# Performance work log

Measured on AMD Instinct MI355X. Metric: run time of the kernel, lower is better.

Reference implementation:

```python
import jax, jax.numpy as jnp
import numpy as np

EPS = 1e-5
TOP_K = 2


def _dwconv3x3(x, w):
    # depthwise 3x3, stride 1, padding 1 (SAME)
    return jax.lax.conv_general_dilated(
        x, w, window_strides=(1, 1), padding='SAME',
        feature_group_count=x.shape[1],
        dimension_numbers=('NCHW', 'OIHW', 'NCHW'))


def _bn(x, g, b, m, v):
    # inference-mode BatchNorm2d
    s = g / jnp.sqrt(v + EPS)
    return x * s[None, :, None, None] + (b - m * s)[None, :, None, None]


def setup_inputs() -> dict:
    key = jax.random.key(0)
    ks = jax.random.split(key, 26)
    Bsz, D, H = 16, 384, 32
    S, E, HID = 64, 8, 768
    n, u = jax.random.normal, jax.random.uniform
    inp = {}
    inp['x'] = n(ks[0], (Bsz, D, H, H), jnp.float32)
    inp['dw1_w'] = n(ks[1], (D, 1, 3, 3)) * 0.1
    inp['bn1_g'] = u(ks[2], (D,), minval=0.5, maxval=1.5)
    inp['bn1_b'] = n(ks[3], (D,)) * 0.1
    inp['bn1_m'] = n(ks[4], (D,)) * 0.1
    inp['bn1_v'] = u(ks[5], (D,), minval=0.5, maxval=1.5)
    inp['dw2_w'] = n(ks[6], (D, 1, 3, 3)) * 0.1
    inp['bn2_g'] = u(ks[7], (D,), minval=0.5, maxval=1.5)
    inp['bn2_b'] = n(ks[8], (D,)) * 0.1
    inp['bn2_m'] = n(ks[9], (D,)) * 0.1
    inp['bn2_v'] = u(ks[10], (D,), minval=0.5, maxval=1.5)
    inp['ln_w'] = u(ks[11], (D,), minval=0.5, maxval=1.5)
    inp['ln_b'] = n(ks[12], (D,)) * 0.1
    inp['bcdt_w'] = n(ks[13], (3 * S, D)) * 0.02
    inp['dws_w'] = n(ks[14], (3 * S, 1, 3, 3)) * 0.1
    inp['hproj_w'] = n(ks[15], (D, D)) * 0.02
    inp['A'] = u(ks[16], (S,), minval=1.0, maxval=16.0)
    inp['gate_w'] = n(ks[17], (E, D)) * 0.02
    inp['gate_b'] = n(ks[18], (E,)) * 0.02
    inp['w1'] = n(ks[19], (E, HID, D)) * 0.02
    inp['b1'] = n(ks[20], (E, HID)) * 0.02
    inp['w2'] = n(ks[21], (E, D, HID)) * 0.02
    inp['b2'] = n(ks[22], (E, D)) * 0.02
    inp['w3'] = n(ks[23], (E, HID, D)) * 0.02
    inp['b3'] = n(ks[24], (E, HID)) * 0.02
    return inp


def reference(x, dw1_w, bn1_g, bn1_b, bn1_m, bn1_v, dw2_w, bn2_g, bn2_b, bn2_m,
              bn2_v, ln_w, ln_b, bcdt_w, dws_w, hproj_w, A, gate_w, gate_b,
              w1, b1, w2, b2, w3, b3):
    Bsz, D, H, W = x.shape
    L = H * W
    S = A.shape[0]
    E = gate_w.shape[0]
    # x = x + dwconv1(x)
    x = x + _bn(_dwconv3x3(x, dw1_w), bn1_g, bn1_b, bn1_m, bn1_v)
    x_prev = x
    # LayerNorm1D over channel dim of (B, C, L)
    xf = x.reshape(Bsz, D, L)
    mu = xf.mean(axis=1, keepdims=True)
    var = xf.var(axis=1, keepdims=True)
    xn = (xf - mu) / jnp.sqrt(var + EPS) * ln_w[None, :, None] + ln_b[None, :, None]
    # Slim_SSD mixer
    bcdt = jnp.einsum('cd,bdl->bcl', bcdt_w, xn)            # 1x1 conv1d
    bcdt = _dwconv3x3(bcdt.reshape(Bsz, 3 * S, H, W), dws_w).reshape(Bsz, 3 * S, L)
    Bm, Cm, dt = jnp.split(bcdt, 3, axis=1)                  # each (B, S, L)
    Am = jax.nn.softmax(dt + A[None, :, None], axis=-1)      # softmax over L
    h = jnp.einsum('bdl,bsl->bds', xn, Am * Bm)              # (B, D, S)
    h = jax.nn.silu(jnp.einsum('ed,bds->bes', hproj_w, h))   # h_proj + SiLU
    y = jnp.einsum('bes,bsl->bel', h, Cm).reshape(Bsz, D, H, W)
    x = x_prev + y
    # x = x + dwconv2(x)
    x = x + _bn(_dwconv3x3(x, dw2_w), bn2_g, bn2_b, bn2_m, bn2_v)
    # SparseMoE (TopkRouter, eval mode, filter_radio=0 -> mask==1, bias buffer==0)
    t = x.transpose(0, 2, 3, 1).reshape(-1, D)               # (N, D) tokens
    N = t.shape[0]
    logits = t @ gate_w.T + gate_b                           # (N, E)
    vals, idx = jax.lax.top_k(logits, TOP_K)
    probs = jax.nn.softmax(vals, axis=1)                     # softmax over top-k logits
    wfull = jnp.zeros((N, E), t.dtype).at[jnp.arange(N)[:, None], idx].set(probs)
    ymoe = jnp.zeros_like(t)
    for e in range(E):
        he = jax.nn.silu(t @ w1[e].T + b1[e]) * (t @ w3[e].T + b3[e])
        ymoe = ymoe + (he @ w2[e].T + b2[e]) * wfull[:, e:e + 1]
    x = x + ymoe.reshape(Bsz, H, W, D).transpose(0, 3, 1, 2)
    # dropout is identity in eval mode
    return (x, h)
```

## Files before the change

kernel.cpp:

```cpp
#include <hip/hip_runtime.h>
#include <hip/hip_bf16.h>

#define BSZ 16
#define DCH 384
#define LSP 1024
#define SST 64
#define NEXP 8
#define HID 768
#define NTOK 16384
#define MOE_MAXT 520

#define OFF_X1    0ULL
#define OFF_XN    25165824ULL
#define OFF_BCDT  50331648ULL
#define OFF_BCDTC 62914560ULL
#define OFF_H     75497472ULL
#define OFF_X2    77070336ULL
#define OFF_META  102236160ULL
#define OFF_LOGITS (OFF_META)
#define OFF_PROBS  (OFF_META +  524288ULL)
#define OFF_IDX    (OFF_META +  655360ULL)
#define OFF_CNT    (OFF_META +  786432ULL)
#define OFF_FILL   (OFF_META +  786464ULL)
#define OFF_OFFS   (OFF_META +  786496ULL)
#define OFF_TOFF   (OFF_META +  786560ULL)
#define OFF_LTOK   (OFF_META +  786624ULL)
#define OFF_LP     (OFF_META +  917696ULL)
#define OFF_TPOS   (OFF_META + 1048768ULL)
#define OFF_HE    0ULL
#define OFF_T16   OFF_BCDT
#define OFF_W1B   OFF_BCDTC
#define OFF_W3B   (OFF_BCDTC + 4718592ULL)
#define OFF_W2B   (OFF_BCDTC + 9437184ULL)
#define OFF_YMOE  OFF_X2
#define OFF_HPRE  OFF_X2

typedef __attribute__((ext_vector_type(8))) short bf16x8;
typedef __attribute__((ext_vector_type(4))) float f32x4;
typedef __attribute__((ext_vector_type(4))) unsigned short u16x4;

__device__ __forceinline__ unsigned short f2bf(float f) {
  union { float f; unsigned int u; } x; x.f = f;
  unsigned int r = (x.u + 0x7fffu + ((x.u >> 16) & 1u)) >> 16;
  return (unsigned short)r;
}
__device__ __forceinline__ float bf2f(unsigned short s) {
  union { unsigned int u; float f; } x; x.u = ((unsigned int)s) << 16; return x.f;
}

__global__ void k_dwbnres(const float* __restrict__ x, const float* __restrict__ w,
                          const float* __restrict__ g, const float* __restrict__ bb,
                          const float* __restrict__ mm, const float* __restrict__ vv,
                          float* __restrict__ out, int C) {
  int bc = blockIdx.x;
  int c = bc % C;
  __shared__ float tile[34 * 34];
  const float* img = x + (size_t)bc * 1024;
  for (int i = threadIdx.x; i < 34 * 34; i += 256) tile[i] = 0.f;
  __syncthreads();
  for (int i = threadIdx.x; i < 1024; i += 256) {
    int r = i >> 5, cc = i & 31;
    tile[(r + 1) * 34 + (cc + 1)] = img[i];
  }
  __syncthreads();
  float w0 = w[c*9+0], w1 = w[c*9+1], w2 = w[c*9+2], w3 = w[c*9+3], w4 = w[c*9+4],
        w5 = w[c*9+5], w6 = w[c*9+6], w7 = w[c*9+7], w8 = w[c*9+8];
  bool res = (g != nullptr);
  float scale = 1.f, bias = 0.f;
  if (res) { float s = g[c] * rsqrtf(vv[c] + 1e-5f); scale = s; bias = bb[c] - mm[c] * s; }
  for (int i = threadIdx.x; i < 1024; i += 256) {
    int r = i >> 5, cc = i & 31;
    const float* t0 = &tile[r * 34 + cc];
    float acc = t0[0]*w0 + t0[1]*w1 + t0[2]*w2
              + t0[34]*w3 + t0[35]*w4 + t0[36]*w5
              + t0[68]*w6 + t0[69]*w7 + t0[70]*w8;
    float o = res ? (t0[35] + acc * scale + bias) : acc;
    out[(size_t)bc * 1024 + i] = o;
  }
}

__global__ void k_layernorm(const float* __restrict__ x, const float* __restrict__ lw,
                            const float* __restrict__ lb, float* __restrict__ xn) {
  int lane = threadIdx.x & 63;
  int slice = threadIdx.x >> 6;
  int pos0 = blockIdx.x * 64;
  int b = pos0 >> 10;
  int l = (pos0 & 1023) + lane;
  const float* xb = x + (size_t)b * DCH * LSP + l;
  float s = 0.f, s2 = 0.f;
  for (int d = slice * 96; d < slice * 96 + 96; d++) {
    float v = xb[(size_t)d * LSP];
    s += v; s2 += v * v;
  }
  __shared__ float red[2][4][64];
  red[0][slice][lane] = s; red[1][slice][lane] = s2;
  __syncthreads();
  if (slice == 0) {
    s  = red[0][0][lane] + red[0][1][lane] + red[0][2][lane] + red[0][3][lane];
    s2 = red[1][0][lane] + red[1][1][lane] + red[1][2][lane] + red[1][3][lane];
    float mu = s * (1.f / 384.f);
    float var = s2 * (1.f / 384.f) - mu * mu;
    red[0][0][lane] = mu;
    red[1][0][lane] = rsqrtf(var + 1e-5f);
  }
  __syncthreads();
  float mu = red[0][0][lane], rs = red[1][0][lane];
  float* xnb = xn + (size_t)b * DCH * LSP + l;
  for (int d = slice * 96; d < slice * 96 + 96; d++) {
    float v = xb[(size_t)d * LSP];
    xnb[(size_t)d * LSP] = (v - mu) * rs * lw[d] + lb[d];
  }
}

__global__ void k_bcdt(const float* __restrict__ xn, const float* __restrict__ wt,
                       float* __restrict__ out) {
  int lt = blockIdx.x, ct = blockIdx.y, b = blockIdx.z;
  __shared__ float wsm[64][33];
  __shared__ float xs[32][129];
  int lg = threadIdx.x & 31, cg = threadIdx.x >> 5;
  float acc[8][4];
  for (int i = 0; i < 8; i++) for (int j = 0; j < 4; j++) acc[i][j] = 0.f;
  const float* xb = xn + (size_t)b * DCH * LSP + lt * 128;
  for (int d0 = 0; d0 < 384; d0 += 32) {
    for (int i = threadIdx.x; i < 2048; i += 256) {
      int c = i >> 5, dd = i & 31;
      wsm[c][dd] = wt[(size_t)(ct * 64 + c) * 384 + d0 + dd];
    }
    for (int i = threadIdx.x; i < 4096; i += 256) {
      int dd = i >> 7, ll = i & 127;
      xs[dd][ll] = xb[(size_t)(d0 + dd) * LSP + ll];
    }
    __syncthreads();
    for (int dd = 0; dd < 32; dd++) {
      float xv[4];
      #pragma unroll
      for (int il = 0; il < 4; il++) xv[il] = xs[dd][lg + 32 * il];
      #pragma unroll
      for (int ic = 0; ic < 8; ic++) {
        float wv = wsm[cg + 8 * ic][dd];
        #pragma unroll
        for (int il = 0; il < 4; il++) acc[ic][il] += wv * xv[il];
      }
    }
    __syncthreads();
  }
  for (int ic = 0; ic < 8; ic++)
    for (int il = 0; il < 4; il++)
      out[(size_t)b * 196608 + (size_t)(ct * 64 + cg + 8 * ic) * 1024 + lt * 128 + lg + 32 * il] = acc[ic][il];
}

__global__ void k_softmax(float* __restrict__ bc, const float* __restrict__ Av) {
  int b = blockIdx.x >> 6, s = blockIdx.x & 63;
  float* row = bc + (size_t)b * 196608 + (size_t)(128 + s) * 1024;
  float a = Av[s];
  int t = threadIdx.x;
  float v[4]; float mx = -3.0e38f;
  #pragma unroll
  for (int i = 0; i < 4; i++) { v[i] = row[t + 256 * i] + a; mx = fmaxf(mx, v[i]); }
  #pragma unroll
  for (int off = 32; off >= 1; off >>= 1) mx = fmaxf(mx, __shfl_xor(mx, off));
  __shared__ float redm[4], reds[4];
  if ((t & 63) == 0) redm[t >> 6] = mx;
  __syncthreads();
  mx = fmaxf(fmaxf(redm[0], redm[1]), fmaxf(redm[2], redm[3]));
  float sm = 0.f;
  #pragma unroll
  for (int i = 0; i < 4; i++) { v[i] = __expf(v[i] - mx); sm += v[i]; }
  #pragma unroll
  for (int off = 32; off >= 1; off >>= 1) sm += __shfl_xor(sm, off);
  if ((t & 63) == 0) reds[t >> 6] = sm;
  __syncthreads();
  sm = reds[0] + reds[1] + reds[2] + reds[3];
  float inv = 1.f / sm;
  #pragma unroll
  for (int i = 0; i < 4; i++) row[t + 256 * i] = v[i] * inv;
}

__global__ void k_h(const float* __restrict__ xn, const float* __restrict__ bc,
                    float* __restrict__ h) {
  int dt_ = blockIdx.x, ls = blockIdx.y, b = blockIdx.z;
  __shared__ float xs[64][65];
  __shared__ float ab[64][65];
  int tid = threadIdx.x;
  int sg4 = tid & 15, dg4 = tid >> 4;
  float acc[4][4];
  #pragma unroll
  for (int i = 0; i < 4; i++)
    #pragma unroll
    for (int j = 0; j < 4; j++) acc[i][j] = 0.f;
  const float* Bm = bc + (size_t)b * 196608;
  const float* Am = Bm + 131072;
  const float* xb = xn + (size_t)b * DCH * LSP + (size_t)(dt_ * 64) * LSP;
  for (int l0 = ls * 128; l0 < ls * 128 + 128; l0 += 64) {
    for (int i = tid; i < 4096; i += 256) {
      int r = i >> 6, ll = i & 63;
      xs[r][ll] = xb[(size_t)r * LSP + l0 + ll];
      ab[r][ll] = Am[(size_t)r * 1024 + l0 + ll] * Bm[(size_t)r * 1024 + l0 + ll];
    }
    __syncthreads();
    for (int ll = 0; ll < 64; ll++) {
      float xv[4], av[4];
      #pragma unroll
      for (int i = 0; i < 4; i++) xv[i] = xs[dg4 * 4 + i][ll];
      #pragma unroll
      for (int j = 0; j < 4; j++) av[j] = ab[sg4 * 4 + j][ll];
      #pragma unroll
      for (int i = 0; i < 4; i++)
        #pragma unroll
        for (int j = 0; j < 4; j++) acc[i][j] += xv[i] * av[j];
    }
    __syncthreads();
  }
  float* hb = h + (size_t)b * DCH * SST + (size_t)(dt_ * 64) * 64;
  #pragma unroll
  for (int i = 0; i < 4; i++)
    #pragma unroll
    for (int j = 0; j < 4; j++)
      atomicAdd(&hb[(size_t)(dg4 * 4 + i) * 64 + sg4 * 4 + j], acc[i][j]);
}

__global__ void k_hproj(const float* __restrict__ h, const float* __restrict__ pw,
                        float* __restrict__ hpre) {
  int et = blockIdx.x, ks = blockIdx.y, b = blockIdx.z;
  __shared__ float hs[64][65];
  __shared__ float ps[64][65];
  int tid = threadIdx.x;
  int sg4 = tid & 15, eg4 = tid >> 4;
  float acc[4][4];
  #pragma unroll
  for (int i = 0; i < 4; i++)
    #pragma unroll
    for (int j = 0; j < 4; j++) acc[i][j] = 0.f;
  for (int d0 = ks * 128; d0 < ks * 128 + 128; d0 += 64) {
    for (int i = tid; i < 4096; i += 256) {
      int r = i >> 6, cc = i & 63;
      hs[r][cc] = h[(size_t)b * DCH * SST + (size_t)(d0 + r) * 64 + cc];
      ps[r][cc] = pw[(size_t)(et * 64 + r) * 384 + d0 + cc];
    }
    __syncthreads();
    for (int dd = 0; dd < 64; dd++) {
      float pv[4], hv[4];
      #pragma unroll
      for (int i = 0; i < 4; i++) pv[i] = ps[eg4 * 4 + i][dd];
      #pragma unroll
      for (int j = 0; j < 4; j++) hv[j] = hs[dd][sg4 * 4 + j];
      #pragma unroll
      for (int i = 0; i < 4; i++)
        #pragma unroll
        for (int j = 0; j < 4; j++) acc[i][j] += pv[i] * hv[j];
    }
    __syncthreads();
  }
  float* hb = hpre + (size_t)b * DCH * SST + (size_t)(et * 64) * 64;
  #pragma unroll
  for (int i = 0; i < 4; i++)
    #pragma unroll
    for (int j = 0; j < 4; j++)
      atomicAdd(&hb[(size_t)(eg4 * 4 + i) * 64 + sg4 * 4 + j], acc[i][j]);
}

__global__ void k_silu(const float* __restrict__ hpre, float* __restrict__ h2) {
  int i = blockIdx.x * 256 + threadIdx.x;
  float4 v = ((const float4*)hpre)[i];
  v.x = v.x / (1.f + __expf(-v.x));
  v.y = v.y / (1.f + __expf(-v.y));
  v.z = v.z / (1.f + __expf(-v.z));
  v.w = v.w / (1.f + __expf(-v.w));
  ((float4*)h2)[i] = v;
}

__global__ void k_y(const float* __restrict__ h2, const float* __restrict__ bc,
                    const float* __restrict__ x1, float* __restrict__ x2) {
  int lt = blockIdx.x, dt_ = blockIdx.y, b = blockIdx.z;
  __shared__ float hss[32][65];
  __shared__ float cs[64][129];
  int lg = threadIdx.x & 31, dg = threadIdx.x >> 5;
  float acc[4][4];
  for (int i = 0; i < 4; i++) for (int j = 0; j < 4; j++) acc[i][j] = 0.f;
  for (int i = threadIdx.x; i < 2048; i += 256) {
    int r = i >> 6, cc = i & 63;
    hss[r][cc] = h2[(size_t)b * DCH * SST + (size_t)(dt_ * 32 + r) * 64 + cc];
  }
  const float* Cm = bc + (size_t)b * 196608 + 65536;
  for (int i = threadIdx.x; i < 8192; i += 256) {
    int ss = i >> 7, ll = i & 127;
    cs[ss][ll] = Cm[(size_t)ss * 1024 + lt * 128 + ll];
  }
  __syncthreads();
  for (int ss = 0; ss < 64; ss++) {
    float cv[4];
    #pragma unroll
    for (int il = 0; il < 4; il++) cv[il] = cs[ss][lg + 32 * il];
    #pragma unroll
    for (int id = 0; id < 4; id++) {
      float hv = hss[dg * 4 + id][ss];
      #pragma unroll
      for (int il = 0; il < 4; il++) acc[id][il] += hv * cv[il];
    }
  }
  size_t base = (size_t)b * DCH * LSP + (size_t)(dt_ * 32) * LSP + lt * 128;
  for (int id = 0; id < 4; id++)
    for (int il = 0; il < 4; il++) {
      size_t o = base + (size_t)(dg * 4 + id) * LSP + lg + 32 * il;
      x2[o] = x1[o] + acc[id][il];
    }
}

__global__ void k_router(const float* __restrict__ x3, const float* __restrict__ gw,
                         const float* __restrict__ gb, float* __restrict__ logits) {
  __shared__ float xs[64][65];
  __shared__ float gs[8][64];
  int blk = blockIdx.x;
  int b = blk >> 4; int l0 = (blk & 15) * 64;
  int lg = threadIdx.x & 63, eg = threadIdx.x >> 6;
  float acc0 = 0.f, acc1 = 0.f;
  const float* xb = x3 + (size_t)b * DCH * LSP + l0;
  for (int d0 = 0; d0 < 384; d0 += 64) {
    for (int i = threadIdx.x; i < 4096; i += 256) {
      int dd = i >> 6, ll = i & 63;
      xs[dd][ll] = xb[(size_t)(d0 + dd) * LSP + ll];
    }
    for (int i = threadIdx.x; i < 512; i += 256) {
      int e = i >> 6, dd = i & 63;
      gs[e][dd] = gw[(size_t)e * 384 + d0 + dd];
    }
    __syncthreads();
    for (int dd = 0; dd < 64; dd++) {
      float xv = xs[dd][lg];
      acc0 += gs[eg][dd] * xv;
      acc1 += gs[eg + 4][dd] * xv;
    }
    __syncthreads();
  }
  int n = b * 1024 + l0 + lg;
  logits[(size_t)n * 8 + eg]     = acc0 + gb[eg];
  logits[(size_t)n * 8 + eg + 4] = acc1 + gb[eg + 4];
}

__global__ void k_topk(const float* __restrict__ logits, float* __restrict__ probs,
                       int* __restrict__ idx, int* __restrict__ cnt) {
  __shared__ int lcnt[8];
  if (threadIdx.x < 8) lcnt[threadIdx.x] = 0;
  __syncthreads();
  int n = blockIdx.x * 256 + threadIdx.x;
  float lv[8];
  for (int e = 0; e < 8; e++) lv[e] = logits[(size_t)n * 8 + e];
  int i1 = 0; float v1 = lv[0];
  for (int e = 1; e < 8; e++) if (lv[e] > v1) { v1 = lv[e]; i1 = e; }
  int i2 = -1; float v2 = -3.0e38f;
  for (int e = 0; e < 8; e++) { if (e == i1) continue; if (lv[e] > v2) { v2 = lv[e]; i2 = e; } }
  float p1 = 1.f / (1.f + __expf(v2 - v1));
  probs[n * 2] = p1; probs[n * 2 + 1] = 1.f - p1;
  idx[n * 2] = i1; idx[n * 2 + 1] = i2;
  atomicAdd(&lcnt[i1], 1); atomicAdd(&lcnt[i2], 1);
  __syncthreads();
  if (threadIdx.x < 8) atomicAdd(&cnt[threadIdx.x], lcnt[threadIdx.x]);
}

__global__ void k_offsets(const int* __restrict__ cnt, int* __restrict__ offs,
                          int* __restrict__ toff) {
  if (threadIdx.x == 0) {
    int a = 0, t = 0;
    for (int e = 0; e < 8; e++) {
      offs[e] = a; toff[e] = t;
      a += cnt[e]; t += (cnt[e] + 63) >> 6;
    }
    toff[8] = t;
  }
}

__global__ void k_build(const int* __restrict__ idx, const float* __restrict__ probs,
                        const int* __restrict__ offs, int* __restrict__ fill,
                        int* __restrict__ ltok, float* __restrict__ lp,
                        int* __restrict__ tpos) {
  __shared__ int lcnt[8], lbase[8];
  if (threadIdx.x < 8) lcnt[threadIdx.x] = 0;
  __syncthreads();
  int n = blockIdx.x * 256 + threadIdx.x;
  int e0 = idx[n * 2], e1 = idx[n * 2 + 1];
  int o0 = atomicAdd(&lcnt[e0], 1);
  int o1 = atomicAdd(&lcnt[e1], 1);
  __syncthreads();
  if (threadIdx.x < 8) lbase[threadIdx.x] = atomicAdd(&fill[threadIdx.x], lcnt[threadIdx.x]);
  __syncthreads();
  int p0 = offs[e0] + lbase[e0] + o0;
  int p1 = offs[e1] + lbase[e1] + o1;
  ltok[p0] = n; lp[p0] = probs[n * 2];     tpos[n * 2] = p0;
  ltok[p1] = n; lp[p1] = probs[n * 2 + 1]; tpos[n * 2 + 1] = p1;
}

__global__ void k_t16(const float* __restrict__ x3, unsigned short* __restrict__ t16) {
  __shared__ float tl[32][33];
  int lt = blockIdx.x, dt_ = blockIdx.y, b = blockIdx.z;
  const float* xb = x3 + (size_t)b * DCH * LSP + (size_t)(dt_ * 32) * LSP + lt * 32;
  for (int i = threadIdx.x; i < 1024; i += 256) {
    int dd = i >> 5, ll = i & 31;
    tl[dd][ll] = xb[(size_t)dd * LSP + ll];
  }
  __syncthreads();
  for (int i = threadIdx.x; i < 1024; i += 256) {
    int ll = i >> 5, dd = i & 31;
    int n = b * 1024 + lt * 32 + ll;
    t16[(size_t)n * 384 + dt_ * 32 + dd] = f2bf(tl[dd][ll]);
  }
}

__global__ void k_f2bf3(const float* __restrict__ s0, const float* __restrict__ s1,
                        const float* __restrict__ s2, unsigned short* __restrict__ d0,
                        unsigned short* __restrict__ d1, unsigned short* __restrict__ d2,
                        int n4) {
  int i = blockIdx.x * 256 + threadIdx.x;
  if (i >= n4) return;
  const float* s = (blockIdx.y == 0) ? s0 : (blockIdx.y == 1) ? s1 : s2;
  unsigned short* d = (blockIdx.y == 0) ? d0 : (blockIdx.y == 1) ? d1 : d2;
  float4 v = ((const float4*)s)[i];
  u16x4 o;
  o.x = f2bf(v.x); o.y = f2bf(v.y); o.z = f2bf(v.z); o.w = f2bf(v.w);
  ((u16x4*)d)[i] = o;
}

__global__ void __launch_bounds__(256) k_moe1(
    const unsigned short* __restrict__ t16, const unsigned short* __restrict__ w1,
    const unsigned short* __restrict__ w3, const float* __restrict__ b1,
    const float* __restrict__ b3, const int* __restrict__ ltok,
    const int* __restrict__ cnt, const int* __restrict__ offs,
    const int* __restrict__ toff, unsigned short* __restrict__ he) {
  int tb = blockIdx.x;
  if (tb >= toff[8]) return;
  int e = 0;
  #pragma unroll
  for (int i = 1; i < 8; i++) if (toff[i] <= tb) e = i;
  int rt = tb - toff[e];
  int ne = cnt[e], base = offs[e];
  int ct = blockIdx.y;
  __shared__ unsigned short As[64 * 40];
  __shared__ unsigned short B1s[128 * 40], B3s[128 * 40];
  __shared__ int toks[64];
  int tid = threadIdx.x;
  if (tid < 64) {
    int r = rt * 64 + tid;
    toks[tid] = ltok[base + (r < ne ? r : ne - 1)];
  }
  __syncthreads();
  int lane = tid & 63, wave = tid >> 6;
  int wm = (wave & 1) * 32, wn = (wave >> 1) * 64;
  int fm = lane & 15, fq = lane >> 4;
  f32x4 acc1[2][4], acc3[2][4];
  #pragma unroll
  for (int mi = 0; mi < 2; mi++)
    #pragma unroll
    for (int ni = 0; ni < 4; ni++) { acc1[mi][ni] = (f32x4)(0.f); acc3[mi][ni] = (f32x4)(0.f); }
  int lrow = tid >> 2, lkk = (tid & 3) * 8;
  const unsigned short* w1e = w1 + ((size_t)e * 768 + ct * 128) * 384;
  const unsigned short* w3e = w3 + ((size_t)e * 768 + ct * 128) * 384;
  size_t arow = (size_t)toks[lrow] * 384;
  for (int k0 = 0; k0 < 384; k0 += 32) {
    *(bf16x8*)&As[lrow * 40 + lkk]          = *(const bf16x8*)(t16 + arow + k0 + lkk);
    *(bf16x8*)&B1s[lrow * 40 + lkk]         = *(const bf16x8*)(w1e + (size_t)lrow * 384 + k0 + lkk);
    *(bf16x8*)&B1s[(lrow + 64) * 40 + lkk]  = *(const bf16x8*)(w1e + (size_t)(lrow + 64) * 384 + k0 + lkk);
    *(bf16x8*)&B3s[lrow * 40 + lkk]         = *(const bf16x8*)(w3e + (size_t)lrow * 384 + k0 + lkk);
    *(bf16x8*)&B3s[(lrow + 64) * 40 + lkk]  = *(const bf16x8*)(w3e + (size_t)(lrow + 64) * 384 + k0 + lkk);
    __syncthreads();
    bf16x8 av[2];
    #pragma unroll
    for (int mi = 0; mi < 2; mi++) av[mi] = *(bf16x8*)&As[(wm + mi * 16 + fm) * 40 + fq * 8];
    #pragma unroll
    for (int ni = 0; ni < 4; ni++) {
      bf16x8 b1v = *(bf16x8*)&B1s[(wn + ni * 16 + fm) * 40 + fq * 8];
      bf16x8 b3v = *(bf16x8*)&B3s[(wn + ni * 16 + fm) * 40 + fq * 8];
      #pragma unroll
      for (int mi = 0; mi < 2; mi++) {
        acc1[mi][ni] = __builtin_amdgcn_mfma_f32_16x16x32_bf16(av[mi], b1v, acc1[mi][ni], 0, 0, 0);
        acc3[mi][ni] = __builtin_amdgcn_mfma_f32_16x16x32_bf16(av[mi], b3v, acc3[mi][ni], 0, 0, 0);
      }
    }
    __syncthreads();
  }
  #pragma unroll
  for (int mi = 0; mi < 2; mi++)
    #pragma unroll
    for (int ni = 0; ni < 4; ni++)
      #pragma unroll
      for (int r = 0; r < 4; r++) {
        int lr = wm + mi * 16 + fq * 4 + r;
        int gr = rt * 64 + lr;
        if (gr < ne) {
          int col = ct * 128 + wn + ni * 16 + fm;
          float z1 = acc1[mi][ni][r] + b1[e * 768 + col];
          float z3 = acc3[mi][ni][r] + b3[e * 768 + col];
          float val = (z1 / (1.f + __expf(-z1))) * z3;
          he[((size_t)base + gr) * 768 + col] = f2bf(val);
        }
      }
}

__global__ void __launch_bounds__(256) k_moe2(
    const unsigned short* __restrict__ he, const unsigned short* __restrict__ w2,
    const float* __restrict__ b2, const float* __restrict__ lp,
    const int* __restrict__ cnt, const int* __restrict__ offs,
    const int* __restrict__ toff, unsigned short* __restrict__ ymoe) {
  int tb = blockIdx.x;
  if (tb >= toff[8]) return;
  int e = 0;
  #pragma unroll
  for (int i = 1; i < 8; i++) if (toff[i] <= tb) e = i;
  int rt = tb - toff[e];
  int ne = cnt[e], base = offs[e];
  int ct = blockIdx.y;
  __shared__ unsigned short As[64 * 40];
  __shared__ unsigned short Bs[128 * 40];
  __shared__ float lps[64];
  int tid = threadIdx.x;
  if (tid < 64) {
    int r = rt * 64 + tid;
    lps[tid] = lp[base + (r < ne ? r : ne - 1)];
  }
  int lane = tid & 63, wave = tid >> 6;
  int wm = (wave & 1) * 32, wn = (wave >> 1) * 64;
  int fm = lane & 15, fq = lane >> 4;
  f32x4 acc[2][4];
  #pragma unroll
  for (int mi = 0; mi < 2; mi++)
    #pragma unroll
    for (int ni = 0; ni < 4; ni++) acc[mi][ni] = (f32x4)(0.f);
  int lrow = tid >> 2, lkk = (tid & 3) * 8;
  int ar = base + rt * 64 + lrow; if (ar > 32767) ar = 32767;
  const unsigned short* Arow = he + (size_t)ar * 768;
  const unsigned short* Brow = w2 + ((size_t)e * 384 + ct * 128 + lrow) * 768;
  const unsigned short* Brow2 = Brow + (size_t)64 * 768;
  for (int k0 = 0; k0 < 768; k0 += 32) {
    *(bf16x8*)&As[lrow * 40 + lkk]         = *(const bf16x8*)(Arow + k0 + lkk);
    *(bf16x8*)&Bs[lrow * 40 + lkk]         = *(const bf16x8*)(Brow + k0 + lkk);
    *(bf16x8*)&Bs[(lrow + 64) * 40 + lkk]  = *(const bf16x8*)(Brow2 + k0 + lkk);
    __syncthreads();
    bf16x8 av[2];
    #pragma unroll
    for (int mi = 0; mi < 2; mi++) av[mi] = *(bf16x8*)&As[(wm + mi * 16 + fm) * 40 + fq * 8];
    #pragma unroll
    for (int ni = 0; ni < 4; ni++) {
      bf16x8 bv = *(bf16x8*)&Bs[(wn + ni * 16 + fm) * 40 + fq * 8];
      #pragma unroll
      for (int mi = 0; mi < 2; mi++)
        acc[mi][ni] = __builtin_amdgcn_mfma_f32_16x16x32_bf16(av[mi], bv, acc[mi][ni], 0, 0, 0);
    }
    __syncthreads();
  }
  #pragma unroll
  for (int mi = 0; mi < 2; mi++)
    #pragma unroll
    for (int ni = 0; ni < 4; ni++)
      #pragma unroll
      for (int r = 0; r < 4; r++) {
        int lr = wm + mi * 16 + fq * 4 + r;
        int gr = rt * 64 + lr;
        if (gr < ne) {
          int col = ct * 128 + wn + ni * 16 + fm;
          float val = (acc[mi][ni][r] + b2[e * 384 + col]) * lps[lr];
          ymoe[((size_t)base + gr) * 384 + col] = f2bf(val);
        }
      }
}

__global__ void k_scatter(const unsigned short* __restrict__ ymoe,
                          const int* __restrict__ tpos, float* __restrict__ xout) {
  int dt_ = blockIdx.x;
  int lt = blockIdx.y;
  int b = blockIdx.z;
  int l = threadIdx.x & 63;
  int d0 = dt_ * 32 + (threadIdx.x >> 6) * 8;
  int n = b * 1024 + lt * 64 + l;
  int p0 = tpos[2 * n], p1 = tpos[2 * n + 1];
  bf16x8 y0 = *(const bf16x8*)(ymoe + (size_t)p0 * 384 + d0);
  bf16x8 y1 = *(const bf16x8*)(ymoe + (size_t)p1 * 384 + d0);
  size_t base = (size_t)b * DCH * LSP + (size_t)d0 * LSP + lt * 64 + l;
  #pragma unroll
  for (int k = 0; k < 8; k++) {
    float v = bf2f((unsigned short)y0[k]) + bf2f((unsigned short)y1[k]);
    xout[base + (size_t)k * LSP] += v;
  }
}

extern "C" void kernel_launch(void* const* d_in, const int* in_sizes, int n_in,
                              void* d_out, int out_size, void* d_ws, size_t ws_size,
                              hipStream_t stream) {
  const float* x      = (const float*)d_in[0];
  const float* dw1    = (const float*)d_in[1];
  const float* bn1g   = (const float*)d_in[2];
  const float* bn1b   = (const float*)d_in[3];
  const float* bn1m   = (const float*)d_in[4];
  const float* bn1v   = (const float*)d_in[5];
  const float* dw2    = (const float*)d_in[6];
  const float* bn2g   = (const float*)d_in[7];
  const float* bn2b   = (const float*)d_in[8];
  const float* bn2m   = (const float*)d_in[9];
  const float* bn2v   = (const float*)d_in[10];
  const float* lnw    = (const float*)d_in[11];
  const float* lnb    = (const float*)d_in[12];
  const float* bcdtw  = (const float*)d_in[13];
  const float* dwsw   = (const float*)d_in[14];
  const float* hprojw = (const float*)d_in[15];
  const float* Avec   = (const float*)d_in[16];
  const float* gatew  = (const float*)d_in[17];
  const float* gateb  = (const float*)d_in[18];
  const float* w1f    = (const float*)d_in[19];
  const float* b1f    = (const float*)d_in[20];
  const float* w2f    = (const float*)d_in[21];
  const float* b2f    = (const float*)d_in[22];
  const float* w3f    = (const float*)d_in[23];
  const float* b3f    = (const float*)d_in[24];

  char* wsb = (char*)d_ws;
  float* x1    = (float*)(wsb + OFF_X1);
  float* xn    = (float*)(wsb + OFF_XN);
  float* bcdt  = (float*)(wsb + OFF_BCDT);
  float* bcdtc = (float*)(wsb + OFF_BCDTC);
  float* hbuf  = (float*)(wsb + OFF_H);
  float* hpre  = (float*)(wsb + OFF_HPRE);
  float* x2    = (float*)(wsb + OFF_X2);
  float* logits = (float*)(wsb + OFF_LOGITS);
  float* probs  = (float*)(wsb + OFF_PROBS);
  int*   idx    = (int*)(wsb + OFF_IDX);
  int*   cnt    = (int*)(wsb + OFF_CNT);
  int*   fill   = (int*)(wsb + OFF_FILL);
  int*   offs   = (int*)(wsb + OFF_OFFS);
  int*   toff   = (int*)(wsb + OFF_TOFF);
  int*   ltok   = (int*)(wsb + OFF_LTOK);
  float* lp     = (float*)(wsb + OFF_LP);
  int*   tpos   = (int*)(wsb + OFF_TPOS);
  unsigned short* t16  = (unsigned short*)(wsb + OFF_T16);
  unsigned short* w1b  = (unsigned short*)(wsb + OFF_W1B);
  unsigned short* w3b  = (unsigned short*)(wsb + OFF_W3B);
  unsigned short* w2b  = (unsigned short*)(wsb + OFF_W2B);
  unsigned short* he   = (unsigned short*)(wsb + OFF_HE);
  unsigned short* ymoe = (unsigned short*)(wsb + OFF_YMOE);
  float* xout = (float*)d_out;
  float* h2   = xout + (size_t)BSZ * DCH * LSP;

  k_dwbnres<<<BSZ * DCH, 256, 0, stream>>>(x, dw1, bn1g, bn1b, bn1m, bn1v, x1, DCH);
  k_layernorm<<<NTOK / 64, 256, 0, stream>>>(x1, lnw, lnb, xn);
  k_bcdt<<<dim3(8, 3, BSZ), 256, 0, stream>>>(xn, bcdtw, bcdt);
  k_dwbnres<<<BSZ * 192, 256, 0, stream>>>(bcdt, dwsw, nullptr, nullptr, nullptr, nullptr, bcdtc, 192);
  k_softmax<<<BSZ * SST, 256, 0, stream>>>(bcdtc, Avec);
  hipMemsetAsync(hbuf, 0, (size_t)BSZ * DCH * SST * 4, stream);
  hipMemsetAsync(hpre, 0, (size_t)BSZ * DCH * SST * 4, stream);
  k_h<<<dim3(6, 8, BSZ), 256, 0, stream>>>(xn, bcdtc, hbuf);
  k_hproj<<<dim3(6, 3, BSZ), 256, 0, stream>>>(hbuf, hprojw, hpre);
  k_silu<<<(BSZ * DCH * SST / 4) / 256, 256, 0, stream>>>(hpre, h2);
  k_y<<<dim3(8, 12, BSZ), 256, 0, stream>>>(h2, bcdtc, x1, x2);
  k_dwbnres<<<BSZ * DCH, 256, 0, stream>>>(x2, dw2, bn2g, bn2b, bn2m, bn2v, xout, DCH);
  hipMemsetAsync(wsb + OFF_CNT, 0, 64, stream);
  k_router<<<256, 256, 0, stream>>>(xout, gatew, gateb, logits);
  k_topk<<<NTOK / 256, 256, 0, stream>>>(logits, probs, idx, cnt);
  k_offsets<<<1, 64, 0, stream>>>(cnt, offs, toff);
  k_build<<<NTOK / 256, 256, 0, stream>>>(idx, probs, offs, fill, ltok, lp, tpos);
  k_t16<<<dim3(32, 12, BSZ), 256, 0, stream>>>(xout, t16);
  int n4 = NEXP * HID * DCH / 4;
  k_f2bf3<<<dim3((n4 + 255) / 256, 3), 256, 0, stream>>>(w1f, w3f, w2f, w1b, w3b, w2b, n4);
  k_moe1<<<dim3(MOE_MAXT, 6), 256, 0, stream>>>(t16, w1b, w3b, b1f, b3f, ltok, cnt, offs, toff, he);
  k_moe2<<<dim3(MOE_MAXT, 3), 256, 0, stream>>>(he, w2b, b2f, lp, cnt, offs, toff, ymoe);
  k_scatter<<<dim3(12, 16, BSZ), 256, 0, stream>>>(ymoe, tpos, xout);
}
```

Baseline: 586.7 us.

## Use direct global-to-LDS async loads with XOR swizzle and BK=64 in MoE GEMMs

Both MoE expert GEMM kernels now stage A and B tiles with global_load_lds, which writes global memory straight into LDS and skips the trip through registers. The K step grows from 32 to 64, and the LDS layout changes from padded rows to an XOR-swizzled 64-wide layout to avoid bank conflicts. The goal is to cut load instruction overhead, halve the number of barriers, and reduce register pressure. The risks are that the async loads may not be properly waited on before the barrier, and that the larger LDS footprint lowers occupancy.

```diff
diff --git a/kernel.cpp b/kernel.cpp
--- a/kernel.cpp
+++ b/kernel.cpp
@@ -48,6 +48,15 @@
   union { unsigned int u; float f; } x; x.u = ((unsigned int)s) << 16; return x.f;
 }
 
+__device__ __forceinline__ void async16(const void* g, void* l) {
+  unsigned long long gi = reinterpret_cast<unsigned long long>(g);
+  unsigned int li = (unsigned int)reinterpret_cast<unsigned long long>(l);
+  __builtin_amdgcn_global_load_lds(
+      (const __attribute__((address_space(1))) unsigned int*)gi,
+      (__attribute__((address_space(3))) unsigned int*)(unsigned long long)li,
+      16, 0, 0);
+}
+
 __global__ void k_dwbnres(const float* __restrict__ x, const float* __restrict__ w,
                           const float* __restrict__ g, const float* __restrict__ bb,
                           const float* __restrict__ mm, const float* __restrict__ vv,
@@ -433,8 +442,9 @@
   int rt = tb - toff[e];
   int ne = cnt[e], base = offs[e];
   int ct = blockIdx.y;
-  __shared__ unsigned short As[64 * 40];
-  __shared__ unsigned short B1s[128 * 40], B3s[128 * 40];
+  __shared__ unsigned short As[64 * 64];
+  __shared__ unsigned short B1s[128 * 64];
+  __shared__ unsigned short B3s[128 * 64];
   __shared__ int toks[64];
   int tid = threadIdx.x;
   if (tid < 64) {
@@ -445,33 +455,56 @@
   int lane = tid & 63, wave = tid >> 6;
   int wm = (wave & 1) * 32, wn = (wave >> 1) * 64;
   int fm = lane & 15, fq = lane >> 4;
+  int srow = lane >> 3, slot = lane & 7;
   f32x4 acc1[2][4], acc3[2][4];
   #pragma unroll
   for (int mi = 0; mi < 2; mi++)
     #pragma unroll
     for (int ni = 0; ni < 4; ni++) { acc1[mi][ni] = (f32x4)(0.f); acc3[mi][ni] = (f32x4)(0.f); }
-  int lrow = tid >> 2, lkk = (tid & 3) * 8;
   const unsigned short* w1e = w1 + ((size_t)e * 768 + ct * 128) * 384;
   const unsigned short* w3e = w3 + ((size_t)e * 768 + ct * 128) * 384;
-  size_t arow = (size_t)toks[lrow] * 384;
-  for (int k0 = 0; k0 < 384; k0 += 32) {
-    *(bf16x8*)&As[lrow * 40 + lkk]          = *(const bf16x8*)(t16 + arow + k0 + lkk);
-    *(bf16x8*)&B1s[lrow * 40 + lkk]         = *(const bf16x8*)(w1e + (size_t)lrow * 384 + k0 + lkk);
-    *(bf16x8*)&B1s[(lrow + 64) * 40 + lkk]  = *(const bf16x8*)(w1e + (size_t)(lrow + 64) * 384 + k0 + lkk);
-    *(bf16x8*)&B3s[lrow * 40 + lkk]         = *(const bf16x8*)(w3e + (size_t)lrow * 384 + k0 + lkk);
-    *(bf16x8*)&B3s[(lrow + 64) * 40 + lkk]  = *(const bf16x8*)(w3e + (size_t)(lrow + 64) * 384 + k0 + lkk);
-    __syncthreads();
-    bf16x8 av[2];
-    #pragma unroll
-    for (int mi = 0; mi < 2; mi++) av[mi] = *(bf16x8*)&As[(wm + mi * 16 + fm) * 40 + fq * 8];
-    #pragma unroll
-    for (int ni = 0; ni < 4; ni++) {
-      bf16x8 b1v = *(bf16x8*)&B1s[(wn + ni * 16 + fm) * 40 + fq * 8];
-      bf16x8 b3v = *(bf16x8*)&B3s[(wn + ni * 16 + fm) * 40 + fq * 8];
+  int ar0 = wave * 16 + srow, ar1 = wave * 16 + 8 + srow;
+  const unsigned short* ag0 = t16 + (size_t)toks[ar0] * 384 + ((slot ^ (ar0 & 7)) * 8);
+  const unsigned short* ag1 = t16 + (size_t)toks[ar1] * 384 + ((slot ^ (ar1 & 7)) * 8);
+  const unsigned short* b1g[4]; const unsigned short* b3g[4];
+  #pragma unroll
+  for (int ii = 0; ii < 4; ii++) {
+    int brow = wave * 32 + ii * 8 + srow;
+    int coff = (slot ^ (brow & 7)) * 8;
+    b1g[ii] = w1e + (size_t)brow * 384 + coff;
+    b3g[ii] = w3e + (size_t)brow * 384 + coff;
+  }
+  unsigned short* asw0 = &As[(wave * 16) * 64];
+  unsigned short* asw1 = &As[(wave * 16 + 8) * 64];
+  for (int k0 = 0; k0 < 384; k0 += 64) {
+    async16(ag0 + k0, asw0);
+    async16(ag1 + k0, asw1);
+    #pragma unroll
+    for (int ii = 0; ii < 4; ii++) {
+      async16(b1g[ii] + k0, &B1s[(wave * 32 + ii * 8) * 64]);
+      async16(b3g[ii] + k0, &B3s[(wave * 32 + ii * 8) * 64]);
+    }
+    __syncthreads();
+    #pragma unroll
+    for (int kk = 0; kk < 2; kk++) {
+      int c = kk * 4 + fq;
+      bf16x8 av[2];
       #pragma unroll
       for (int mi = 0; mi < 2; mi++) {
-        acc1[mi][ni] = __builtin_amdgcn_mfma_f32_16x16x32_bf16(av[mi], b1v, acc1[mi][ni], 0, 0, 0);
-        acc3[mi][ni] = __builtin_amdgcn_mfma_f32_16x16x32_bf16(av[mi], b3v, acc3[mi][ni], 0, 0, 0);
+        int row = wm + mi * 16 + fm;
+        av[mi] = *(bf16x8*)&As[row * 64 + ((c ^ (row & 7)) * 8)];
+      }
+      #pragma unroll
+      for (int ni = 0; ni < 4; ni++) {
+        int row = wn + ni * 16 + fm;
+        int off = row * 64 + ((c ^ (row & 7)) * 8);
+        bf16x8 b1v = *(bf16x8*)&B1s[off];
+        bf16x8 b3v = *(bf16x8*)&B3s[off];
+        #pragma unroll
+        for (int mi = 0; mi < 2; mi++) {
+          acc1[mi][ni] = __builtin_amdgcn_mfma_f32_16x16x32_bf16(av[mi], b1v, acc1[mi][ni], 0, 0, 0);
+          acc3[mi][ni] = __builtin_amdgcn_mfma_f32_16x16x32_bf16(av[mi], b3v, acc3[mi][ni], 0, 0, 0);
+        }
       }
     }
     __syncthreads();
@@ -507,8 +540,8 @@
   int rt = tb - toff[e];
   int ne = cnt[e], base = offs[e];
   int ct = blockIdx.y;
-  __shared__ unsigned short As[64 * 40];
-  __shared__ unsigned short Bs[128 * 40];
+  __shared__ unsigned short As[64 * 64];
+  __shared__ unsigned short Bs[128 * 64];
   __shared__ float lps[64];
   int tid = threadIdx.x;
   if (tid < 64) {
@@ -518,30 +551,50 @@
   int lane = tid & 63, wave = tid >> 6;
   int wm = (wave & 1) * 32, wn = (wave >> 1) * 64;
   int fm = lane & 15, fq = lane >> 4;
+  int srow = lane >> 3, slot = lane & 7;
   f32x4 acc[2][4];
   #pragma unroll
   for (int mi = 0; mi < 2; mi++)
     #pragma unroll
     for (int ni = 0; ni < 4; ni++) acc[mi][ni] = (f32x4)(0.f);
-  int lrow = tid >> 2, lkk = (tid & 3) * 8;
-  int ar = base + rt * 64 + lrow; if (ar > 32767) ar = 32767;
-  const unsigned short* Arow = he + (size_t)ar * 768;
-  const unsigned short* Brow = w2 + ((size_t)e * 384 + ct * 128 + lrow) * 768;
-  const unsigned short* Brow2 = Brow + (size_t)64 * 768;
-  for (int k0 = 0; k0 < 768; k0 += 32) {
-    *(bf16x8*)&As[lrow * 40 + lkk]         = *(const bf16x8*)(Arow + k0 + lkk);
-    *(bf16x8*)&Bs[lrow * 40 + lkk]         = *(const bf16x8*)(Brow + k0 + lkk);
-    *(bf16x8*)&Bs[(lrow + 64) * 40 + lkk]  = *(const bf16x8*)(Brow2 + k0 + lkk);
-    __syncthreads();
-    bf16x8 av[2];
-    #pragma unroll
-    for (int mi = 0; mi < 2; mi++) av[mi] = *(bf16x8*)&As[(wm + mi * 16 + fm) * 40 + fq * 8];
-    #pragma unroll
-    for (int ni = 0; ni < 4; ni++) {
-      bf16x8 bv = *(bf16x8*)&Bs[(wn + ni * 16 + fm) * 40 + fq * 8];
-      #pragma unroll
-      for (int mi = 0; mi < 2; mi++)
-        acc[mi][ni] = __builtin_amdgcn_mfma_f32_16x16x32_bf16(av[mi], bv, acc[mi][ni], 0, 0, 0);
+  const unsigned short* w2e = w2 + ((size_t)e * 384 + ct * 128) * 768;
+  int ar0 = wave * 16 + srow, ar1 = wave * 16 + 8 + srow;
+  int g0 = base + rt * 64 + ar0; if (g0 > 32767) g0 = 32767;
+  int g1 = base + rt * 64 + ar1; if (g1 > 32767) g1 = 32767;
+  const unsigned short* ag0 = he + (size_t)g0 * 768 + ((slot ^ (ar0 & 7)) * 8);
+  const unsigned short* ag1 = he + (size_t)g1 * 768 + ((slot ^ (ar1 & 7)) * 8);
+  const unsigned short* bg[4];
+  #pragma unroll
+  for (int ii = 0; ii < 4; ii++) {
+    int brow = wave * 32 + ii * 8 + srow;
+    bg[ii] = w2e + (size_t)brow * 768 + ((slot ^ (brow & 7)) * 8);
+  }
+  unsigned short* asw0 = &As[(wave * 16) * 64];
+  unsigned short* asw1 = &As[(wave * 16 + 8) * 64];
+  for (int k0 = 0; k0 < 768; k0 += 64) {
+    async16(ag0 + k0, asw0);
+    async16(ag1 + k0, asw1);
+    #pragma unroll
+    for (int ii = 0; ii < 4; ii++)
+      async16(bg[ii] + k0, &Bs[(wave * 32 + ii * 8) * 64]);
+    __syncthreads();
+    #pragma unroll
+    for (int kk = 0; kk < 2; kk++) {
+      int c = kk * 4 + fq;
+      bf16x8 av[2];
+      #pragma unroll
+      for (int mi = 0; mi < 2; mi++) {
+        int row = wm + mi * 16 + fm;
+        av[mi] = *(bf16x8*)&As[row * 64 + ((c ^ (row & 7)) * 8)];
+      }
+      #pragma unroll
+      for (int ni = 0; ni < 4; ni++) {
+        int row = wn + ni * 16 + fm;
+        bf16x8 bv = *(bf16x8*)&Bs[row * 64 + ((c ^ (row & 7)) * 8)];
+        #pragma unroll
+        for (int mi = 0; mi < 2; mi++)
+          acc[mi][ni] = __builtin_amdgcn_mfma_f32_16x16x32_bf16(av[mi], bv, acc[mi][ni], 0, 0, 0);
+      }
     }
     __syncthreads();
   }
```

New measurement: 554.1 us. 1.06x faster.
